# Kernel tuning notes

Hardware: AMD Instinct MI355X
Metric: run time of the kernel (lower is better)

The kernel has to match this reference:

```python
import jax, jax.numpy as jnp
import numpy as np

B, N, H, D, E = 32, 1000, 256, 128, 512000
NB = B * N


def setup_inputs() -> dict:
    key = jax.random.key(0)
    ks = jax.random.split(key, 16)
    s = 0.05
    inp = {
        "x": jax.random.normal(ks[0], (B, D), jnp.float32),
        "h_prev": jax.random.normal(ks[1], (B, N, H), jnp.float32),
        "c_prev": jax.random.normal(ks[2], (B, N, H), jnp.float32),
        "src": jax.random.randint(ks[3], (E,), 0, NB, jnp.int32),
        "dst": jax.random.randint(ks[4], (E,), 0, NB, jnp.int32),
        "Wi": jax.random.normal(ks[5], (D, H), jnp.float32) * s,
        "bi": jax.random.normal(ks[6], (H,), jnp.float32) * s,
        "Wf": jax.random.normal(ks[7], (D, H), jnp.float32) * s,
        "bf": jax.random.normal(ks[8], (H,), jnp.float32) * s,
        "Wo": jax.random.normal(ks[9], (D, H), jnp.float32) * s,
        "bo": jax.random.normal(ks[10], (H,), jnp.float32) * s,
        "Wc": jax.random.normal(ks[11], (D, H), jnp.float32) * s,
        "bc": jax.random.normal(ks[12], (H,), jnp.float32) * s,
        "Wg": jax.random.normal(ks[13], (H, H), jnp.float32) * s,
        "bg": jax.random.normal(ks[14], (H,), jnp.float32) * s,
    }
    return inp


def _graph_conv(src, dst, h, Wg, bg):
    # DGL GraphConv, norm='both': D_dst^{-1/2} * sum_edges (D_src^{-1/2} * h_src) @ W + b
    nb = h.shape[0]
    ones = jnp.ones(src.shape[0], h.dtype)
    deg_out = jnp.maximum(jax.ops.segment_sum(ones, src, num_segments=nb), 1.0)
    deg_in = jnp.maximum(jax.ops.segment_sum(ones, dst, num_segments=nb), 1.0)
    h = h * (deg_out ** -0.5)[:, None]          # pre-normalize by src out-degree
    agg = jax.ops.segment_sum(h[src], dst, num_segments=nb)  # irregular gather/scatter
    agg = agg * (deg_in ** -0.5)[:, None]       # post-normalize by dst in-degree
    return agg @ Wg + bg


def reference(x, h_prev, c_prev, src, dst, Wi, bi, Wf, bf, Wo, bo, Wc, bc, Wg, bg):
    b, n, hh = h_prev.shape
    h_conv = _graph_conv(src, dst, h_prev.reshape(b * n, hh), Wg, bg).reshape(b, n, hh)
    # four input-gate projections, broadcast over nodes
    xi = (x @ Wi + bi)[:, None, :]
    xf = (x @ Wf + bf)[:, None, :]
    xo = (x @ Wo + bo)[:, None, :]
    xc = (x @ Wc + bc)[:, None, :]
    i_t = jax.nn.sigmoid(xi + h_conv)
    f_t = jax.nn.sigmoid(xf + h_conv)
    o_t = jax.nn.sigmoid(xo + h_conv)
    c_tilde = jnp.tanh(xc + h_conv)
    c_t = f_t * c_prev + i_t * c_tilde
    h_t = o_t * jnp.tanh(c_t)
    return h_t, c_t
```

## Files before the change

kernel.cpp:

```cpp
#include <hip/hip_runtime.h>

#define BB 32
#define NN 1000
#define HH 256
#define DD 128
#define EE 512000
#define NB (BB * NN)
#define NBKT 250
#define BKTCAP 2560
#define EPB 2000
#define NP1 256
#define PADS 64

#define GCURD_OFF 0
#define GCURS_OFF (NBKT)
#define DEGI_OFF 512
#define DSOF_OFF (512 + NB)
#define DSIF_OFF (512 + 2 * NB)
#define GATE_OFF (512 + 3 * NB)
#define WGB_OFF (GATE_OFF + 4 * BB * HH)
#define DSTB_OFF (WGB_OFF + (HH * HH) / 2)
#define SRCB_OFF (DSTB_OFF + NBKT * BKTCAP)
#define PAD_OFF (SRCB_OFF + NBKT * BKTCAP / 2)
#define HW_OFF (PAD_OFF + NB * PADS / 2)

using bf16x8 = __attribute__((ext_vector_type(8))) short;
using f32x4 = __attribute__((ext_vector_type(4))) float;

__device__ inline unsigned short f2bf(float x) {
    unsigned u = __float_as_uint(x);
    return (unsigned short)((u + 0x7FFFu + ((u >> 16) & 1u)) >> 16);
}
__device__ inline float bf2f(unsigned short u) {
    return __uint_as_float(((unsigned)u) << 16);
}

__global__ __launch_bounds__(256) void k_prep(
    const float* __restrict__ Wg, unsigned short* __restrict__ wgb,
    int* __restrict__ gcur, const float* __restrict__ x,
    const float* __restrict__ Wi, const float* __restrict__ bi,
    const float* __restrict__ Wf, const float* __restrict__ bf_,
    const float* __restrict__ Wo, const float* __restrict__ bo,
    const float* __restrict__ Wc, const float* __restrict__ bc,
    float* __restrict__ gates) {
    int blk = blockIdx.x;
    int t = threadIdx.x;
    if (blk < 256) {
        int o = blk * 256 + t;
        int j = o & 7;
        int c = o >> 3;
        int lane = c & 63;
        int nt = (c >> 6) & 15;
        int kk = c >> 10;
        int k = kk * 32 + (lane >> 4) * 8 + j;
        int n = nt * 16 + (lane & 15);
        wgb[o] = f2bf(Wg[k * HH + n]);
    } else if (blk < 256 + BB) {
        __shared__ float xs[DD];
        int b = blk - 256;
        if (t < DD) xs[t] = x[b * DD + t];
        __syncthreads();
        float ai = bi[t], af = bf_[t], ao = bo[t], ac = bc[t];
#pragma unroll 4
        for (int k = 0; k < DD; k++) {
            float xv = xs[k];
            ai += xv * Wi[k * HH + t];
            af += xv * Wf[k * HH + t];
            ao += xv * Wo[k * HH + t];
            ac += xv * Wc[k * HH + t];
        }
        gates[0 * BB * HH + b * HH + t] = ai;
        gates[1 * BB * HH + b * HH + t] = af;
        gates[2 * BB * HH + b * HH + t] = ao;
        gates[3 * BB * HH + b * HH + t] = ac;
    } else {
        gcur[t] = 0;
        gcur[256 + t] = 0;
    }
}

__global__ __launch_bounds__(256) void k_main(
    const int* __restrict__ src, const int* __restrict__ dst,
    int* __restrict__ gcurD, int* __restrict__ gcurS,
    unsigned* __restrict__ dstb, unsigned short* __restrict__ srcb,
    const float* __restrict__ h, const unsigned short* __restrict__ wgb,
    unsigned short* __restrict__ hw) {
    int blk = blockIdx.x;
    int t = threadIdx.x;
    if (blk < NB / 64) {
        int lane = t & 63;
        int w = t >> 6;
        int quad = lane >> 4;
        int mrow = lane & 15;
        int r0 = blk * 64 + w * 16;
        int row = r0 + mrow;

        f32x4 acc[16];
#pragma unroll
        for (int nt = 0; nt < 16; nt++) acc[nt] = (f32x4){0.f, 0.f, 0.f, 0.f};

#pragma unroll 1
        for (int kk = 0; kk < 8; kk++) {
            const float* ap = h + (size_t)row * HH + kk * 32 + quad * 8;
            float4 a0 = *(const float4*)ap;
            float4 a1 = *(const float4*)(ap + 4);
            bf16x8 af;
            af[0] = (short)f2bf(a0.x);
            af[1] = (short)f2bf(a0.y);
            af[2] = (short)f2bf(a0.z);
            af[3] = (short)f2bf(a0.w);
            af[4] = (short)f2bf(a1.x);
            af[5] = (short)f2bf(a1.y);
            af[6] = (short)f2bf(a1.z);
            af[7] = (short)f2bf(a1.w);
#pragma unroll
            for (int nt = 0; nt < 16; nt++) {
                bf16x8 bfr =
                    *(const bf16x8*)(wgb + (((kk * 16 + nt) * 64 + lane) << 3));
                acc[nt] = __builtin_amdgcn_mfma_f32_16x16x32_bf16(af, bfr,
                                                                  acc[nt], 0,
                                                                  0, 0);
            }
        }
#pragma unroll
        for (int nt = 0; nt < 16; nt++) {
#pragma unroll
            for (int reg = 0; reg < 4; reg++) {
                hw[(size_t)(r0 + quad * 4 + reg) * HH + nt * 16 + mrow] =
                    f2bf(acc[nt][reg]);
            }
        }
    } else {
        __shared__ int cntD[NBKT], cntS[NBKT], posD[NBKT], posS[NBKT];
        int pb = blk - NB / 64;
        int e0 = pb * EPB;
        for (int i = t; i < NBKT; i += 256) {
            cntD[i] = 0;
            cntS[i] = 0;
        }
        __syncthreads();
        for (int i = t; i < EPB; i += 256) {
            int s = src[e0 + i];
            int d = dst[e0 + i];
            atomicAdd(&cntS[s >> 7], 1);
            atomicAdd(&cntD[d >> 7], 1);
        }
        __syncthreads();
        for (int i = t; i < NBKT; i += 256) {
            posD[i] = atomicAdd(&gcurD[i], cntD[i]);
            posS[i] = atomicAdd(&gcurS[i], cntS[i]);
        }
        __syncthreads();
        for (int i = t; i < EPB; i += 256) {
            int s = src[e0 + i];
            int d = dst[e0 + i];
            int bd = d >> 7, bs = s >> 7;
            int pd = atomicAdd(&posD[bd], 1);
            int ps = atomicAdd(&posS[bs], 1);
            dstb[bd * BKTCAP + pd] = ((unsigned)s << 16) | (unsigned)d;
            srcb[bs * BKTCAP + ps] = (unsigned short)s;
        }
    }
}

__global__ __launch_bounds__(256) void k_csr(
    const int* __restrict__ gcurD, const int* __restrict__ gcurS,
    const unsigned* __restrict__ dstb, const unsigned short* __restrict__ srcb,
    unsigned short* __restrict__ pad16, int* __restrict__ deg_in,
    float* __restrict__ dsif, float* __restrict__ dsof) {
    int blk = blockIdx.x;
    int t = threadIdx.x;
    if (blk < NBKT) {
        __shared__ unsigned short lpad[128 * PADS];
        __shared__ int lcnt[128];
        int qb = blk;
        if (t < 128) lcnt[t] = 0;
        __syncthreads();
        int n = gcurD[qb];
        const unsigned* eb = dstb + qb * BKTCAP;
        for (int i = t; i < n; i += 256) {
            unsigned p = eb[i];
            int s = (int)(p >> 16);
            int dl = (int)(p & 127u);
            int q = atomicAdd(&lcnt[dl], 1);
            if (q < PADS) lpad[dl * PADS + q] = (unsigned short)s;
        }
        __syncthreads();
        int* gp = (int*)(pad16 + (size_t)qb * 128 * PADS);
        const int* lp = (const int*)lpad;
        for (int i = t; i < 128 * PADS / 2; i += 256) gp[i] = lp[i];
        if (t < 128) {
            int c = lcnt[t];
            deg_in[qb * 128 + t] = c;
            dsif[qb * 128 + t] = rsqrtf((float)max(c, 1));
        }
    } else {
        __shared__ int scnt[128];
        int qb = blk - NBKT;
        if (t < 128) scnt[t] = 0;
        __syncthreads();
        int n = gcurS[qb];
        const unsigned short* sb = srcb + qb * BKTCAP;
        for (int i = t; i < n; i += 256) atomicAdd(&scnt[sb[i] & 127], 1);
        __syncthreads();
        if (t < 128) dsof[qb * 128 + t] = rsqrtf((float)max(scnt[t], 1));
    }
}

__device__ inline void lstm1(float hc, float gi, float gf, float go, float gc,
                             float cp, float& ho, float& co) {
    float pi = gi + hc, pf = gf + hc, po = go + hc, pc = gc + hc;
    float it = 1.f / (1.f + __expf(-pi));
    float ft = 1.f / (1.f + __expf(-pf));
    float ot = 1.f / (1.f + __expf(-po));
    float e2 = __expf(2.f * pc);
    float ctl = (e2 - 1.f) / (e2 + 1.f);
    float ct = ft * cp + it * ctl;
    float e2c = __expf(2.f * ct);
    ho = ot * (e2c - 1.f) / (e2c + 1.f);
    co = ct;
}

__global__ __launch_bounds__(256) void k_out(
    const unsigned short* __restrict__ hw,
    const unsigned short* __restrict__ pad16, const int* __restrict__ deg_in,
    const float* __restrict__ dsif, const float* __restrict__ dsof,
    const float* __restrict__ bg, const float* __restrict__ gates,
    const float* __restrict__ c_prev, float* __restrict__ h_out,
    float* __restrict__ c_out) {
    int t = threadIdx.x;
    int lane = t & 63;
    int w = t >> 6;
    int node = blockIdx.x * 4 + w;
    float si = dsif[node];
    int cnt = min(deg_in[node], PADS);
    const unsigned short* pl = pad16 + (size_t)node * PADS;
    int col = lane * 4;
    const unsigned short* hwc = hw + col;

    float ax = 0.f, ay = 0.f, az = 0.f, aw = 0.f;
    int e = 0;
    for (; e + 8 <= cnt; e += 8) {
        ushort4 sa = *(const ushort4*)(pl + e);
        ushort4 sb = *(const ushort4*)(pl + e + 4);
        int s0 = sa.x, s1 = sa.y, s2 = sa.z, s3 = sa.w;
        int s4 = sb.x, s5 = sb.y, s6 = sb.z, s7 = sb.w;
        float c0 = dsof[s0];
        float c1 = dsof[s1];
        float c2 = dsof[s2];
        float c3 = dsof[s3];
        float c4 = dsof[s4];
        float c5 = dsof[s5];
        float c6 = dsof[s6];
        float c7 = dsof[s7];
        ushort4 q0 = *(const ushort4*)(hwc + ((size_t)s0 << 8));
        ushort4 q1 = *(const ushort4*)(hwc + ((size_t)s1 << 8));
        ushort4 q2 = *(const ushort4*)(hwc + ((size_t)s2 << 8));
        ushort4 q3 = *(const ushort4*)(hwc + ((size_t)s3 << 8));
        ushort4 q4 = *(const ushort4*)(hwc + ((size_t)s4 << 8));
        ushort4 q5 = *(const ushort4*)(hwc + ((size_t)s5 << 8));
        ushort4 q6 = *(const ushort4*)(hwc + ((size_t)s6 << 8));
        ushort4 q7 = *(const ushort4*)(hwc + ((size_t)s7 << 8));
        ax += ((c0 * bf2f(q0.x) + c1 * bf2f(q1.x)) +
               (c2 * bf2f(q2.x) + c3 * bf2f(q3.x))) +
              ((c4 * bf2f(q4.x) + c5 * bf2f(q5.x)) +
               (c6 * bf2f(q6.x) + c7 * bf2f(q7.x)));
        ay += ((c0 * bf2f(q0.y) + c1 * bf2f(q1.y)) +
               (c2 * bf2f(q2.y) + c3 * bf2f(q3.y))) +
              ((c4 * bf2f(q4.y) + c5 * bf2f(q5.y)) +
               (c6 * bf2f(q6.y) + c7 * bf2f(q7.y)));
        az += ((c0 * bf2f(q0.z) + c1 * bf2f(q1.z)) +
               (c2 * bf2f(q2.z) + c3 * bf2f(q3.z))) +
              ((c4 * bf2f(q4.z) + c5 * bf2f(q5.z)) +
               (c6 * bf2f(q6.z) + c7 * bf2f(q7.z)));
        aw += ((c0 * bf2f(q0.w) + c1 * bf2f(q1.w)) +
               (c2 * bf2f(q2.w) + c3 * bf2f(q3.w))) +
              ((c4 * bf2f(q4.w) + c5 * bf2f(q5.w)) +
               (c6 * bf2f(q6.w) + c7 * bf2f(q7.w)));
    }
    for (; e < cnt; e++) {
        int s = pl[e];
        float cc = dsof[s];
        ushort4 q = *(const ushort4*)(hwc + ((size_t)s << 8));
        ax += cc * bf2f(q.x);
        ay += cc * bf2f(q.y);
        az += cc * bf2f(q.z);
        aw += cc * bf2f(q.w);
    }

    int b = node / NN;
    float4 bgv = *(const float4*)(bg + col);
    float4 gi = *(const float4*)(gates + 0 * BB * HH + b * HH + col);
    float4 gf = *(const float4*)(gates + 1 * BB * HH + b * HH + col);
    float4 go = *(const float4*)(gates + 2 * BB * HH + b * HH + col);
    float4 gc = *(const float4*)(gates + 3 * BB * HH + b * HH + col);
    float4 cp = *(const float4*)(c_prev + (size_t)node * HH + col);

    float4 ho, co;
    lstm1(ax * si + bgv.x, gi.x, gf.x, go.x, gc.x, cp.x, ho.x, co.x);
    lstm1(ay * si + bgv.y, gi.y, gf.y, go.y, gc.y, cp.y, ho.y, co.y);
    lstm1(az * si + bgv.z, gi.z, gf.z, go.z, gc.z, cp.z, ho.z, co.z);
    lstm1(aw * si + bgv.w, gi.w, gf.w, go.w, gc.w, cp.w, ho.w, co.w);

    *(float4*)(h_out + (size_t)node * HH + col) = ho;
    *(float4*)(c_out + (size_t)node * HH + col) = co;
}

extern "C" void kernel_launch(void* const* d_in, const int* in_sizes, int n_in,
                              void* d_out, int out_size, void* d_ws,
                              size_t ws_size, hipStream_t stream) {
    const float* x = (const float*)d_in[0];
    const float* h_prev = (const float*)d_in[1];
    const float* c_prev = (const float*)d_in[2];
    const int* src = (const int*)d_in[3];
    const int* dst = (const int*)d_in[4];
    const float* Wi = (const float*)d_in[5];
    const float* bi = (const float*)d_in[6];
    const float* Wf = (const float*)d_in[7];
    const float* bf_ = (const float*)d_in[8];
    const float* Wo = (const float*)d_in[9];
    const float* bo = (const float*)d_in[10];
    const float* Wc = (const float*)d_in[11];
    const float* bc = (const float*)d_in[12];
    const float* Wg = (const float*)d_in[13];
    const float* bg = (const float*)d_in[14];

    int* wsi = (int*)d_ws;
    float* wsf = (float*)d_ws;
    int* gcurD = wsi + GCURD_OFF;
    int* gcurS = wsi + GCURS_OFF;
    int* deg_in = wsi + DEGI_OFF;
    float* dsof = wsf + DSOF_OFF;
    float* dsif = wsf + DSIF_OFF;
    float* gates = wsf + GATE_OFF;
    unsigned short* wgb = (unsigned short*)(wsi + WGB_OFF);
    unsigned* dstb = (unsigned*)(wsi + DSTB_OFF);
    unsigned short* srcb = (unsigned short*)(wsi + SRCB_OFF);
    unsigned short* pad16 = (unsigned short*)(wsi + PAD_OFF);
    unsigned short* hw = (unsigned short*)(wsi + HW_OFF);
    float* h_out = (float*)d_out;
    float* c_out = h_out + (size_t)NB * HH;

    k_prep<<<256 + BB + 1, 256, 0, stream>>>(Wg, wgb, gcurD, x, Wi, bi, Wf,
                                             bf_, Wo, bo, Wc, bc, gates);
    k_main<<<NB / 64 + NP1, 256, 0, stream>>>(src, dst, gcurD, gcurS, dstb,
                                              srcb, h_prev, wgb, hw);
    k_csr<<<2 * NBKT, 256, 0, stream>>>(gcurD, gcurS, dstb, srcb, pad16,
                                        deg_in, dsif, dsof);
    k_out<<<NB / 4, 256, 0, stream>>>(hw, pad16, deg_in, dsif, dsof, bg,
                                      gates, c_prev, h_out, c_out);
}
```

Measured before the change: 239.9 us.

## Remap output kernel so each wave gathers 8 nodes over a 32-column slice

The gather/output kernel used to give each wave one destination node across all 256 columns. It now gives each 8-lane group one node and a 32-column slice, so a wave works on 8 nodes at once and 8 consecutive blocks cover the full row. The edge loop unroll drops from 8 to 4. The aim is more independent irregular gathers in flight per wave, to better hide latency from uneven degrees. In exchange, each edge now reads only 64-byte contiguous pieces, and the neighbour index and degree-scale loads are repeated for every column slice.

```diff
diff --git a/kernel.cpp b/kernel.cpp
--- a/kernel.cpp
+++ b/kernel.cpp
@@ -229,54 +229,39 @@
     const float* __restrict__ c_prev, float* __restrict__ h_out,
     float* __restrict__ c_out) {
     int t = threadIdx.x;
+    int w = t >> 6;
     int lane = t & 63;
-    int w = t >> 6;
-    int node = blockIdx.x * 4 + w;
+    int g = lane >> 3;
+    int slice = blockIdx.x & 7;
+    int node = (blockIdx.x >> 3) * 32 + w * 8 + g;
+    int col = slice * 32 + (lane & 7) * 4;
+
     float si = dsif[node];
     int cnt = min(deg_in[node], PADS);
     const unsigned short* pl = pad16 + (size_t)node * PADS;
-    int col = lane * 4;
     const unsigned short* hwc = hw + col;
 
     float ax = 0.f, ay = 0.f, az = 0.f, aw = 0.f;
     int e = 0;
-    for (; e + 8 <= cnt; e += 8) {
-        ushort4 sa = *(const ushort4*)(pl + e);
-        ushort4 sb = *(const ushort4*)(pl + e + 4);
-        int s0 = sa.x, s1 = sa.y, s2 = sa.z, s3 = sa.w;
-        int s4 = sb.x, s5 = sb.y, s6 = sb.z, s7 = sb.w;
+    for (; e + 4 <= cnt; e += 4) {
+        ushort4 ss = *(const ushort4*)(pl + e);
+        int s0 = ss.x, s1 = ss.y, s2 = ss.z, s3 = ss.w;
         float c0 = dsof[s0];
         float c1 = dsof[s1];
         float c2 = dsof[s2];
         float c3 = dsof[s3];
-        float c4 = dsof[s4];
-        float c5 = dsof[s5];
-        float c6 = dsof[s6];
-        float c7 = dsof[s7];
         ushort4 q0 = *(const ushort4*)(hwc + ((size_t)s0 << 8));
         ushort4 q1 = *(const ushort4*)(hwc + ((size_t)s1 << 8));
         ushort4 q2 = *(const ushort4*)(hwc + ((size_t)s2 << 8));
         ushort4 q3 = *(const ushort4*)(hwc + ((size_t)s3 << 8));
-        ushort4 q4 = *(const ushort4*)(hwc + ((size_t)s4 << 8));
-        ushort4 q5 = *(const ushort4*)(hwc + ((size_t)s5 << 8));
-        ushort4 q6 = *(const ushort4*)(hwc + ((size_t)s6 << 8));
-        ushort4 q7 = *(const ushort4*)(hwc + ((size_t)s7 << 8));
-        ax += ((c0 * bf2f(q0.x) + c1 * bf2f(q1.x)) +
-               (c2 * bf2f(q2.x) + c3 * bf2f(q3.x))) +
-              ((c4 * bf2f(q4.x) + c5 * bf2f(q5.x)) +
-               (c6 * bf2f(q6.x) + c7 * bf2f(q7.x)));
-        ay += ((c0 * bf2f(q0.y) + c1 * bf2f(q1.y)) +
-               (c2 * bf2f(q2.y) + c3 * bf2f(q3.y))) +
-              ((c4 * bf2f(q4.y) + c5 * bf2f(q5.y)) +
-               (c6 * bf2f(q6.y) + c7 * bf2f(q7.y)));
-        az += ((c0 * bf2f(q0.z) + c1 * bf2f(q1.z)) +
-               (c2 * bf2f(q2.z) + c3 * bf2f(q3.z))) +
-              ((c4 * bf2f(q4.z) + c5 * bf2f(q5.z)) +
-               (c6 * bf2f(q6.z) + c7 * bf2f(q7.z)));
-        aw += ((c0 * bf2f(q0.w) + c1 * bf2f(q1.w)) +
-               (c2 * bf2f(q2.w) + c3 * bf2f(q3.w))) +
-              ((c4 * bf2f(q4.w) + c5 * bf2f(q5.w)) +
-               (c6 * bf2f(q6.w) + c7 * bf2f(q7.w)));
+        ax += (c0 * bf2f(q0.x) + c1 * bf2f(q1.x)) +
+              (c2 * bf2f(q2.x) + c3 * bf2f(q3.x));
+        ay += (c0 * bf2f(q0.y) + c1 * bf2f(q1.y)) +
+              (c2 * bf2f(q2.y) + c3 * bf2f(q3.y));
+        az += (c0 * bf2f(q0.z) + c1 * bf2f(q1.z)) +
+              (c2 * bf2f(q2.z) + c3 * bf2f(q3.z));
+        aw += (c0 * bf2f(q0.w) + c1 * bf2f(q1.w)) +
+              (c2 * bf2f(q2.w) + c3 * bf2f(q3.w));
     }
     for (; e < cnt; e++) {
         int s = pl[e];
@@ -347,6 +332,7 @@
                                               srcb, h_prev, wgb, hw);
     k_csr<<<2 * NBKT, 256, 0, stream>>>(gcurD, gcurS, dstb, srcb, pad16,
                                         deg_in, dsif, dsof);
-    k_out<<<NB / 4, 256, 0, stream>>>(hw, pad16, deg_in, dsif, dsof, bg,
-                                      gates, c_prev, h_out, c_out);
-}
+    k_out<<<NB / 4 * 8 / 8, 256, 0, stream>>>(hw, pad16, deg_in, dsif, dsof,
+                                              bg, gates, c_prev, h_out,
+                                              c_out);
+}
```

New measurement: 267.4 us. 1.11x slower.
